# Kernel optimization log

Measured on AMD Instinct MI355X. Metric: run time of the kernel, lower is better.

The kernel has to match this reference:

```python
import jax, jax.numpy as jnp
import numpy as np


def conv1x1(x, w, b):
    # x: [B, Cin, D, H, W], w: [Cout, Cin], b: [Cout]
    return jnp.einsum('bcdhw,oc->bodhw', x, w) + b[None, :, None, None, None]


def setup_inputs() -> dict:
    key = jax.random.key(0)
    ks = jax.random.split(key, 9)
    B, C, D, H, W = 2, 64, 16, 16, 16
    Cc = 64          # context_dim
    C8 = C // 8      # inner attention dim
    s = 0.05
    return {
        'x': jax.random.normal(ks[0], (B, C, D, H, W), jnp.float32),
        'context': jax.random.normal(ks[1], (B, Cc, D, H, W), jnp.float32),
        'Wq': jax.random.normal(ks[2], (C8, C), jnp.float32) * s,
        'bq': jax.random.normal(ks[3], (C8,), jnp.float32) * s,
        'Wk': jax.random.normal(ks[4], (C8, Cc), jnp.float32) * s,
        'bk': jax.random.normal(ks[5], (C8,), jnp.float32) * s,
        'Wv': jax.random.normal(ks[6], (C, Cc), jnp.float32) * s,
        'bv': jax.random.normal(ks[7], (C,), jnp.float32) * s,
        'gamma': jax.random.normal(ks[8], (1,), jnp.float32) * s,
    }


def reference(x, context, Wq, bq, Wk, bk, Wv, bv, gamma):
    B, C, D, H, W = x.shape
    N = D * H * W
    q = conv1x1(x, Wq, bq).reshape(B, -1, N)        # [B, C/8, N]
    k = conv1x1(context, Wk, bk).reshape(B, -1, N)  # [B, C/8, N]
    v = conv1x1(context, Wv, bv).reshape(B, C, N)   # [B, C, N]
    # energy[b, n, m] = q[:, :, n] . k[:, :, m]  (no scaling, as in source)
    energy = jnp.einsum('bcn,bcm->bnm', q, k)       # [B, N, N]
    attn = jax.nn.softmax(energy, axis=-1)
    # out = v @ attn^T : out[b, c, n] = sum_m v[b, c, m] * attn[b, n, m]
    out = jnp.einsum('bcm,bnm->bcn', v, attn).reshape(B, C, D, H, W)
    return gamma[0] * out + x
```

## Files before the change

kernel.cpp:

```cpp
#include <hip/hip_runtime.h>

#define NTOK 4096

typedef __attribute__((ext_vector_type(8))) short short8;
typedef __attribute__((ext_vector_type(4))) float f32x4;
typedef __attribute__((ext_vector_type(4))) unsigned int uint4v;

__device__ __forceinline__ unsigned short f2bf(float f) {
    unsigned u = __float_as_uint(f);
    u += 0x7fffu + ((u >> 16) & 1u);
    return (unsigned short)(u >> 16);
}

__device__ __forceinline__ unsigned int pk2(float lo, float hi) {
    return __builtin_amdgcn_perm(__float_as_uint(hi), __float_as_uint(lo), 0x07060302u);
}

__global__ __launch_bounds__(256) void proj(
    const float* __restrict__ x, const float* __restrict__ ctx,
    const float* __restrict__ Wq, const float* __restrict__ bq,
    const float* __restrict__ Wk, const float* __restrict__ bk,
    const float* __restrict__ Wv, const float* __restrict__ bv,
    unsigned short* __restrict__ qbf, unsigned short* __restrict__ kbf,
    unsigned short* __restrict__ vtp)
{
    __shared__ float sW[16 * 64];
    __shared__ float sB[16];
    int tid  = threadIdx.x;
    int ogrp = blockIdx.z;
    int b    = blockIdx.y;
    int n0   = blockIdx.x * 64;

    if (ogrp == 0) {
        for (int i = tid; i < 1024; i += 256)
            sW[i] = (i < 512) ? Wq[i] : Wk[i - 512];
        if (tid < 16) sB[tid] = (tid < 8) ? bq[tid] : bk[tid - 8];
    } else {
        for (int i = tid; i < 1024; i += 256)
            sW[i] = Wv[(ogrp - 1) * 1024 + i];
        if (tid < 16) sB[tid] = bv[(ogrp - 1) * 16 + tid];
    }
    __syncthreads();

    int nn   = tid & 63;
    int osub = tid >> 6;
    const float* inp = (ogrp == 0 && osub < 2) ? x : ctx;
    const float* ip  = inp + (size_t)b * 64 * NTOK + n0 + nn;

    float a0 = sB[osub * 4 + 0], a1 = sB[osub * 4 + 1];
    float a2 = sB[osub * 4 + 2], a3 = sB[osub * 4 + 3];
#pragma unroll 16
    for (int c = 0; c < 64; ++c) {
        float val = ip[(size_t)c * NTOK];
        a0 += sW[(osub * 4 + 0) * 64 + c] * val;
        a1 += sW[(osub * 4 + 1) * 64 + c] * val;
        a2 += sW[(osub * 4 + 2) * 64 + c] * val;
        a3 += sW[(osub * 4 + 3) * 64 + c] * val;
    }
    float av[4] = {a0, a1, a2, a3};

    if (ogrp == 0) {
        bool isq = osub < 2;
        float sc = isq ? 1.4426950408889634f : 1.0f;
        unsigned short* dst = isq ? qbf : kbf;
        int half = osub & 1;
        ushort4 pk = {f2bf(av[0] * sc), f2bf(av[1] * sc), f2bf(av[2] * sc), f2bf(av[3] * sc)};
        *(ushort4*)&dst[((size_t)b * NTOK + n0 + nn) * 8 + half * 4] = pk;
    } else {
        int cbase = (ogrp - 1) * 16 + osub * 4;
        int m  = n0 + nn;
        int g  = m & ~31;
        int mm = m & 31;
        int p  = ((mm >> 2) & 3) * 8 + (mm >> 4) * 4 + (mm & 3);
#pragma unroll
        for (int j = 0; j < 4; ++j)
            vtp[((size_t)b * 64 + cbase + j) * NTOK + g + p] = f2bf(av[j]);
    }
}

__global__ __launch_bounds__(256, 2) void attn6(
    const unsigned short* __restrict__ qbf, const unsigned short* __restrict__ kbf,
    const unsigned short* __restrict__ vtp,
    float* __restrict__ part)
{
    __shared__ float sO[4][64][64];
    __shared__ float sL[4][64];

    int tid  = threadIdx.x;
    int w    = tid >> 6, lane = tid & 63;
    int n    = lane & 15, quad = lane >> 4;
    int nt   = blockIdx.x;
    int b    = blockIdx.y;
    int qz   = blockIdx.z;
    int n0   = nt * 64;

    const f32x4 z4 = {0.f, 0.f, 0.f, 0.f};
    const short8 z8 = {0, 0, 0, 0, 0, 0, 0, 0};

    short8 bq[4];
#pragma unroll
    for (int g = 0; g < 4; ++g)
        bq[g] = (quad == 0)
            ? *(const short8*)&qbf[((size_t)b * NTOK + n0 + g * 16 + n) * 8]
            : z8;

    const unsigned short* kb = kbf + (size_t)b * NTOK * 8;
    const unsigned short* vb = vtp + (size_t)b * 64 * NTOK;
    int mwbase = qz * 1024 + w * 256;

    f32x4 acc[4][4];
#pragma unroll
    for (int g = 0; g < 4; ++g)
#pragma unroll
        for (int ct = 0; ct < 4; ++ct) acc[g][ct] = z4;
    float lsum[4] = {0.f, 0.f, 0.f, 0.f};

    for (int h = 0; h < 4; ++h) {
        int m0 = mwbase + h * 64;

        short8 kf0 = (quad == 0) ? *(const short8*)&kb[(size_t)(m0 + 0 * 16 + n) * 8] : z8;
        short8 kf1 = (quad == 0) ? *(const short8*)&kb[(size_t)(m0 + 1 * 16 + n) * 8] : z8;
        short8 kf2 = (quad == 0) ? *(const short8*)&kb[(size_t)(m0 + 2 * 16 + n) * 8] : z8;
        short8 kf3 = (quad == 0) ? *(const short8*)&kb[(size_t)(m0 + 3 * 16 + n) * 8] : z8;

        short8 af[2][4];
#pragma unroll
        for (int s = 0; s < 2; ++s)
#pragma unroll
            for (int ct = 0; ct < 4; ++ct)
                af[s][ct] = *(const short8*)&vb[(size_t)(ct * 16 + n) * NTOK
                                                + m0 + s * 32 + quad * 8];

#pragma unroll
        for (int g = 0; g < 4; ++g) {
            f32x4 sa0 = __builtin_amdgcn_mfma_f32_16x16x32_bf16(kf0, bq[g], z4, 0, 0, 0);
            f32x4 sa1 = __builtin_amdgcn_mfma_f32_16x16x32_bf16(kf1, bq[g], z4, 0, 0, 0);
            f32x4 sa2 = __builtin_amdgcn_mfma_f32_16x16x32_bf16(kf2, bq[g], z4, 0, 0, 0);
            f32x4 sa3 = __builtin_amdgcn_mfma_f32_16x16x32_bf16(kf3, bq[g], z4, 0, 0, 0);

            float e00 = __builtin_amdgcn_exp2f(sa0[0]), e01 = __builtin_amdgcn_exp2f(sa0[1]);
            float e02 = __builtin_amdgcn_exp2f(sa0[2]), e03 = __builtin_amdgcn_exp2f(sa0[3]);
            float e10 = __builtin_amdgcn_exp2f(sa1[0]), e11 = __builtin_amdgcn_exp2f(sa1[1]);
            float e12 = __builtin_amdgcn_exp2f(sa1[2]), e13 = __builtin_amdgcn_exp2f(sa1[3]);
            float e20 = __builtin_amdgcn_exp2f(sa2[0]), e21 = __builtin_amdgcn_exp2f(sa2[1]);
            float e22 = __builtin_amdgcn_exp2f(sa2[2]), e23 = __builtin_amdgcn_exp2f(sa2[3]);
            float e30 = __builtin_amdgcn_exp2f(sa3[0]), e31 = __builtin_amdgcn_exp2f(sa3[1]);
            float e32 = __builtin_amdgcn_exp2f(sa3[2]), e33 = __builtin_amdgcn_exp2f(sa3[3]);
            lsum[g] += ((e00 + e01) + (e02 + e03)) + ((e10 + e11) + (e12 + e13))
                     + ((e20 + e21) + (e22 + e23)) + ((e30 + e31) + (e32 + e33));

            uint4v t0, t1;
            t0[0] = pk2(e00, e01); t0[1] = pk2(e02, e03);
            t0[2] = pk2(e10, e11); t0[3] = pk2(e12, e13);
            t1[0] = pk2(e20, e21); t1[1] = pk2(e22, e23);
            t1[2] = pk2(e30, e31); t1[3] = pk2(e32, e33);
            short8 pf0 = __builtin_bit_cast(short8, t0);
            short8 pf1 = __builtin_bit_cast(short8, t1);

            acc[g][0] = __builtin_amdgcn_mfma_f32_16x16x32_bf16(af[0][0], pf0, acc[g][0], 0, 0, 0);
            acc[g][1] = __builtin_amdgcn_mfma_f32_16x16x32_bf16(af[0][1], pf0, acc[g][1], 0, 0, 0);
            acc[g][2] = __builtin_amdgcn_mfma_f32_16x16x32_bf16(af[0][2], pf0, acc[g][2], 0, 0, 0);
            acc[g][3] = __builtin_amdgcn_mfma_f32_16x16x32_bf16(af[0][3], pf0, acc[g][3], 0, 0, 0);
            acc[g][0] = __builtin_amdgcn_mfma_f32_16x16x32_bf16(af[1][0], pf1, acc[g][0], 0, 0, 0);
            acc[g][1] = __builtin_amdgcn_mfma_f32_16x16x32_bf16(af[1][1], pf1, acc[g][1], 0, 0, 0);
            acc[g][2] = __builtin_amdgcn_mfma_f32_16x16x32_bf16(af[1][2], pf1, acc[g][2], 0, 0, 0);
            acc[g][3] = __builtin_amdgcn_mfma_f32_16x16x32_bf16(af[1][3], pf1, acc[g][3], 0, 0, 0);
        }
    }

#pragma unroll
    for (int g = 0; g < 4; ++g) {
        float l = lsum[g];
        l += __shfl_xor(l, 16);
        l += __shfl_xor(l, 32);
        if (lane < 16) sL[w][g * 16 + n] = l;
    }
#pragma unroll
    for (int g = 0; g < 4; ++g)
#pragma unroll
        for (int ct = 0; ct < 4; ++ct)
#pragma unroll
            for (int r = 0; r < 4; ++r)
                sO[w][ct * 16 + quad * 4 + r][g * 16 + n] = acc[g][ct][r];
    __syncthreads();

    float* pb = part + ((size_t)((b * 64 + nt) * 4 + qz)) * 4160;
    for (int i = tid; i < 4096; i += 256) {
        int c = i >> 6, nn2 = i & 63;
        pb[i] = sO[0][c][nn2] + sO[1][c][nn2] + sO[2][c][nn2] + sO[3][c][nn2];
    }
    if (tid < 64)
        pb[4096 + tid] = sL[0][tid] + sL[1][tid] + sL[2][tid] + sL[3][tid];
}

__global__ __launch_bounds__(256) void mergeq(
    const float* __restrict__ part, const float* __restrict__ x,
    const float* __restrict__ gamma, float* __restrict__ out)
{
    int tid = threadIdx.x;
    int nt  = blockIdx.x;
    int b   = blockIdx.y;
    int c   = tid >> 2;
    int j   = tid & 3;

    const float* pb = part + ((size_t)((b * 64 + nt) * 4)) * 4160;
    float g = gamma[0];
#pragma unroll
    for (int nq = 0; nq < 4; ++nq) {
        int ns = j * 16 + nq * 4;
        float4 o = {0.f, 0.f, 0.f, 0.f};
        float4 L = {0.f, 0.f, 0.f, 0.f};
#pragma unroll
        for (int qz = 0; qz < 4; ++qz) {
            const float* p = pb + qz * 4160;
            float4 ov = *(const float4*)&p[c * 64 + ns];
            float4 lv = *(const float4*)&p[4096 + ns];
            o.x += ov.x; o.y += ov.y; o.z += ov.z; o.w += ov.w;
            L.x += lv.x; L.y += lv.y; L.z += lv.z; L.w += lv.w;
        }
        size_t ob = ((size_t)b * 64 + c) * NTOK + nt * 64 + ns;
        float4 xv = *(const float4*)&x[ob];
        float4 res;
        res.x = g * (o.x / L.x) + xv.x;
        res.y = g * (o.y / L.y) + xv.y;
        res.z = g * (o.z / L.z) + xv.z;
        res.w = g * (o.w / L.w) + xv.w;
        *(float4*)&out[ob] = res;
    }
}

extern "C" void kernel_launch(void* const* d_in, const int* in_sizes, int n_in,
                              void* d_out, int out_size, void* d_ws, size_t ws_size,
                              hipStream_t stream) {
    const float* x     = (const float*)d_in[0];
    const float* ctx   = (const float*)d_in[1];
    const float* Wq    = (const float*)d_in[2];
    const float* bq    = (const float*)d_in[3];
    const float* Wk    = (const float*)d_in[4];
    const float* bk    = (const float*)d_in[5];
    const float* Wv    = (const float*)d_in[6];
    const float* bv    = (const float*)d_in[7];
    const float* gamma = (const float*)d_in[8];
    float* out = (float*)d_out;

    unsigned short* qbf = (unsigned short*)d_ws;
    unsigned short* kbf = qbf + 2 * NTOK * 8;
    unsigned short* vtp = kbf + 2 * NTOK * 8;
    float* part = (float*)(vtp + 2 * 64 * NTOK);

    proj<<<dim3(64, 2, 5), 256, 0, stream>>>(x, ctx, Wq, bq, Wk, bk, Wv, bv, qbf, kbf, vtp);
    attn6<<<dim3(NTOK / 64, 2, 4), 256, 0, stream>>>(qbf, kbf, vtp, part);
    mergeq<<<dim3(NTOK / 64, 2), 256, 0, stream>>>(part, x, gamma, out);
}
```

Measured before the change: 111.4 us.

## Split attention keys eight ways, store bf16 partials, shrink LDS staging

Doubles the key-dimension split from 4 to 8 chunks, so the attention grid grows from 512 to 1024 blocks and each block does half the work, which should improve occupancy and latency hiding. Partial outputs are written as bf16 instead of fp32 to keep the added partial traffic manageable. The LDS reduction buffer is shrunk and processed in four channel chunks with extra barriers, which frees shared memory. The costs are a second-level bf16 rounding of the unnormalized partial sums, more barriers, and a merge kernel that reads twice as many partials.

```diff
diff --git a/kernel.cpp b/kernel.cpp
--- a/kernel.cpp
+++ b/kernel.cpp
@@ -10,6 +10,10 @@
     unsigned u = __float_as_uint(f);
     u += 0x7fffu + ((u >> 16) & 1u);
     return (unsigned short)(u >> 16);
+}
+
+__device__ __forceinline__ float bf2f(unsigned short h) {
+    return __uint_as_float((unsigned)h << 16);
 }
 
 __device__ __forceinline__ unsigned int pk2(float lo, float hi) {
@@ -78,12 +82,12 @@
     }
 }
 
-__global__ __launch_bounds__(256, 2) void attn6(
+__global__ __launch_bounds__(256, 2) void attn7(
     const unsigned short* __restrict__ qbf, const unsigned short* __restrict__ kbf,
     const unsigned short* __restrict__ vtp,
-    float* __restrict__ part)
+    unsigned short* __restrict__ partO, float* __restrict__ partL)
 {
-    __shared__ float sO[4][64][64];
+    __shared__ float sOc[4][16][68];
     __shared__ float sL[4][64];
 
     int tid  = threadIdx.x;
@@ -106,7 +110,7 @@
 
     const unsigned short* kb = kbf + (size_t)b * NTOK * 8;
     const unsigned short* vb = vtp + (size_t)b * 64 * NTOK;
-    int mwbase = qz * 1024 + w * 256;
+    int mwbase = qz * 512 + w * 128;
 
     f32x4 acc[4][4];
 #pragma unroll
@@ -115,7 +119,7 @@
         for (int ct = 0; ct < 4; ++ct) acc[g][ct] = z4;
     float lsum[4] = {0.f, 0.f, 0.f, 0.f};
 
-    for (int h = 0; h < 4; ++h) {
+    for (int h = 0; h < 2; ++h) {
         int m0 = mwbase + h * 64;
 
         short8 kf0 = (quad == 0) ? *(const short8*)&kb[(size_t)(m0 + 0 * 16 + n) * 8] : z8;
@@ -175,27 +179,34 @@
         l += __shfl_xor(l, 32);
         if (lane < 16) sL[w][g * 16 + n] = l;
     }
-#pragma unroll
-    for (int g = 0; g < 4; ++g)
-#pragma unroll
-        for (int ct = 0; ct < 4; ++ct)
+
+    unsigned short* pO = partO + ((size_t)((b * 64 + nt) * 8 + qz)) * 4096;
+    float*          pL = partL + ((size_t)((b * 64 + nt) * 8 + qz)) * 64;
+
+#pragma unroll
+    for (int ct = 0; ct < 4; ++ct) {
+        if (ct) __syncthreads();
+#pragma unroll
+        for (int g = 0; g < 4; ++g)
 #pragma unroll
             for (int r = 0; r < 4; ++r)
-                sO[w][ct * 16 + quad * 4 + r][g * 16 + n] = acc[g][ct][r];
-    __syncthreads();
-
-    float* pb = part + ((size_t)((b * 64 + nt) * 4 + qz)) * 4160;
-    for (int i = tid; i < 4096; i += 256) {
-        int c = i >> 6, nn2 = i & 63;
-        pb[i] = sO[0][c][nn2] + sO[1][c][nn2] + sO[2][c][nn2] + sO[3][c][nn2];
+                sOc[w][quad * 4 + r][g * 16 + n] = acc[g][ct][r];
+        __syncthreads();
+        for (int i = tid; i < 1024; i += 256) {
+            int c16 = i >> 6, nn2 = i & 63;
+            float s = sOc[0][c16][nn2] + sOc[1][c16][nn2]
+                    + sOc[2][c16][nn2] + sOc[3][c16][nn2];
+            pO[ct * 1024 + i] = f2bf(s);
+        }
     }
     if (tid < 64)
-        pb[4096 + tid] = sL[0][tid] + sL[1][tid] + sL[2][tid] + sL[3][tid];
+        pL[tid] = sL[0][tid] + sL[1][tid] + sL[2][tid] + sL[3][tid];
 }
 
 __global__ __launch_bounds__(256) void mergeq(
-    const float* __restrict__ part, const float* __restrict__ x,
-    const float* __restrict__ gamma, float* __restrict__ out)
+    const unsigned short* __restrict__ partO, const float* __restrict__ partL,
+    const float* __restrict__ x, const float* __restrict__ gamma,
+    float* __restrict__ out)
 {
     int tid = threadIdx.x;
     int nt  = blockIdx.x;
@@ -203,7 +214,8 @@
     int c   = tid >> 2;
     int j   = tid & 3;
 
-    const float* pb = part + ((size_t)((b * 64 + nt) * 4)) * 4160;
+    const unsigned short* pOb = partO + ((size_t)((b * 64 + nt) * 8)) * 4096;
+    const float*          pLb = partL + ((size_t)((b * 64 + nt) * 8)) * 64;
     float g = gamma[0];
 #pragma unroll
     for (int nq = 0; nq < 4; ++nq) {
@@ -211,11 +223,11 @@
         float4 o = {0.f, 0.f, 0.f, 0.f};
         float4 L = {0.f, 0.f, 0.f, 0.f};
 #pragma unroll
-        for (int qz = 0; qz < 4; ++qz) {
-            const float* p = pb + qz * 4160;
-            float4 ov = *(const float4*)&p[c * 64 + ns];
-            float4 lv = *(const float4*)&p[4096 + ns];
-            o.x += ov.x; o.y += ov.y; o.z += ov.z; o.w += ov.w;
+        for (int qz = 0; qz < 8; ++qz) {
+            ushort4 ov = *(const ushort4*)&pOb[qz * 4096 + c * 64 + ns];
+            float4  lv = *(const float4*)&pLb[qz * 64 + ns];
+            o.x += bf2f(ov.x); o.y += bf2f(ov.y);
+            o.z += bf2f(ov.z); o.w += bf2f(ov.w);
             L.x += lv.x; L.y += lv.y; L.z += lv.z; L.w += lv.w;
         }
         size_t ob = ((size_t)b * 64 + c) * NTOK + nt * 64 + ns;
@@ -243,12 +255,13 @@
     const float* gamma = (const float*)d_in[8];
     float* out = (float*)d_out;
 
-    unsigned short* qbf = (unsigned short*)d_ws;
-    unsigned short* kbf = qbf + 2 * NTOK * 8;
-    unsigned short* vtp = kbf + 2 * NTOK * 8;
-    float* part = (float*)(vtp + 2 * 64 * NTOK);
+    unsigned short* qbf   = (unsigned short*)d_ws;
+    unsigned short* kbf   = qbf + 2 * NTOK * 8;
+    unsigned short* vtp   = kbf + 2 * NTOK * 8;
+    unsigned short* partO = vtp + 2 * 64 * NTOK;
+    float*          partL = (float*)(partO + (size_t)2 * 64 * 8 * 4096);
 
     proj<<<dim3(64, 2, 5), 256, 0, stream>>>(x, ctx, Wq, bq, Wk, bk, Wv, bv, qbf, kbf, vtp);
-    attn6<<<dim3(NTOK / 64, 2, 4), 256, 0, stream>>>(qbf, kbf, vtp, part);
-    mergeq<<<dim3(NTOK / 64, 2), 256, 0, stream>>>(part, x, gamma, out);
-}
+    attn7<<<dim3(NTOK / 64, 2, 8), 256, 0, stream>>>(qbf, kbf, vtp, partO, partL);
+    mergeq<<<dim3(NTOK / 64, 2), 256, 0, stream>>>(partO, partL, x, gamma, out);
+}
```

Result: faster. 100.7 us (-9.6%).
